# Kernel optimization log

Measured on AMD Instinct MI355X. Metric: run time of the kernel, lower is better.

Reference implementation:

```python
import jax, jax.numpy as jnp
import numpy as np

B, N = 1, 512
NODE_DIM, EDGE_DIM = 384, 128
H, SK, SV, PK, PV = 8, 16, 16, 4, 4
EPS = 1e-8
LN_EPS = 1e-5


def setup_inputs() -> dict:
    key = jax.random.key(0)
    ks = jax.random.split(key, 20)
    d, e = NODE_DIM, EDGE_DIM
    s = 0.02
    rn = lambda k, sh: jax.random.normal(k, sh, jnp.float32) * s
    # orthonormal per-residue rotations (valid rigid frames)
    R, _ = jnp.linalg.qr(jax.random.normal(ks[2], (B, N, 3, 3), jnp.float32))
    out_dim = H * (SV + EDGE_DIM + PV * 4)  # scalar + pairwise + points(3) + point norms(1)
    return dict(
        node_features=jax.random.normal(ks[0], (B, N, d), jnp.float32),
        edge_features=jax.random.normal(ks[1], (B, N, N, e), jnp.float32),
        rotations=R,
        translations=jax.random.normal(ks[3], (B, N, 3), jnp.float32),
        mask=jnp.ones((B, N), bool),
        Wq_s=rn(ks[4], (d, H * SK)), Wk_s=rn(ks[5], (d, H * SK)), Wv_s=rn(ks[6], (d, H * SV)),
        Wq_p=rn(ks[7], (d, H * PK * 3)), Wk_p=rn(ks[8], (d, H * PK * 3)), Wv_p=rn(ks[9], (d, H * PV * 3)),
        point_weights=jnp.full((H,), np.log(np.e - 1.0), jnp.float32),  # softplus -> 1
        Wb=rn(ks[10], (e, H)), bb=jnp.zeros((H,), jnp.float32),
        Wo=rn(ks[11], (out_dim, d)), bo=jnp.zeros((d,), jnp.float32),
        g1=jnp.ones((d,), jnp.float32), beta1=jnp.zeros((d,), jnp.float32),
        W1=rn(ks[12], (d, 2 * d)), b1=jnp.zeros((2 * d,), jnp.float32),
        W2=rn(ks[13], (2 * d, 2 * d)), b2=jnp.zeros((2 * d,), jnp.float32),
        W3=rn(ks[14], (2 * d, d)), b3=jnp.zeros((d,), jnp.float32),
        g2=jnp.ones((d,), jnp.float32), beta2=jnp.zeros((d,), jnp.float32),
    )


def _layer_norm(x, g, b):
    mu = x.mean(-1, keepdims=True)
    var = ((x - mu) ** 2).mean(-1, keepdims=True)
    return (x - mu) * jax.lax.rsqrt(var + LN_EPS) * g + b


def _forward(node_features, edge_features, rotations, translations, mask,
             Wq_s, Wk_s, Wv_s, Wq_p, Wk_p, Wv_p, point_weights, Wb, bb, Wo, bo,
             g1, beta1, W1, b1, W2, b2, W3, b3, g2, beta2):
    b, n, d = node_features.shape
    # num_attn_logits = 3 (scalar + point + pairwise)
    scal_scale = (3 * SK) ** -0.5
    point_scale = (3 * PK * 4.5) ** -0.5
    pair_scale = 3 ** -0.5

    qs = (node_features @ Wq_s).reshape(b, n, H, SK)
    kk = (node_features @ Wk_s).reshape(b, n, H, SK)
    vs = (node_features @ Wv_s).reshape(b, n, H, SV)

    def apply_rigid(p):  # p: (b,n,h,d,3); global = R^T applied per lucidrains einsum + t
        return jnp.einsum('bnhdc,bncr->bnhdr', p, rotations) + translations[:, :, None, None, :]

    qp = apply_rigid((node_features @ Wq_p).reshape(b, n, H, PK, 3))
    kp = apply_rigid((node_features @ Wk_p).reshape(b, n, H, PK, 3))
    vp = apply_rigid((node_features @ Wv_p).reshape(b, n, H, PV, 3))

    logits = jnp.einsum('bihk,bjhk->bhij', qs, kk) * scal_scale

    # point distance term: sum_{d,c} (q-k)^2 = |q|^2 + |k|^2 - 2 q.k (avoids (b,h,i,j,d,3) tensor)
    w = jax.nn.softplus(point_weights)  # (H,)
    q2 = jnp.einsum('bnhdc,bnhdc->bhn', qp, qp)
    k2 = jnp.einsum('bnhdc,bnhdc->bhn', kp, kp)
    cross = jnp.einsum('bihdc,bjhdc->bhij', qp, kp)
    dist = q2[..., :, None] + k2[..., None, :] - 2.0 * cross  # (b,h,i,j)
    logits = logits - 0.5 * point_scale * w[None, :, None, None] * dist

    pair_bias = (jnp.einsum('bije,eh->bhij', edge_features, Wb) + bb[None, :, None, None]) * pair_scale
    logits = logits + pair_bias

    pm = mask[:, None, :, None] & mask[:, None, None, :]  # (b,1,i,j)
    logits = jnp.where(pm, logits, -jnp.finfo(logits.dtype).max)
    attn = jax.nn.softmax(logits, axis=-1)  # (b,h,i,j)

    rs = jnp.einsum('bhij,bjhv->bihv', attn, vs).reshape(b, n, H * SV)
    rp = jnp.einsum('bhij,bije->bihe', attn, edge_features).reshape(b, n, H * EDGE_DIM)
    pts = jnp.einsum('bhij,bjhdc->bihdc', attn, vp)
    # invert rigid: subtract t, apply R (inverse of R^T application)
    local = jnp.einsum('bihdc,birc->bihdr', pts - translations[:, :, None, None, :], rotations)
    norms = jnp.sqrt((local ** 2).sum(-1) + EPS)  # (b,n,H,PV)

    cat = jnp.concatenate([rs, local.reshape(b, n, H * PV * 3), norms.reshape(b, n, H * PV), rp], axis=-1)
    ipa_out = cat @ Wo + bo

    x = _layer_norm(ipa_out, g1, beta1)  # dropout is identity at eval
    x = jax.nn.relu(x @ W1 + b1)
    x = jax.nn.relu(x @ W2 + b2)
    x = x @ W3 + b3
    return _layer_norm(x, g2, beta2)


def reference(node_features, edge_features, rotations, translations, mask,
              Wq_s, Wk_s, Wv_s, Wq_p, Wk_p, Wv_p, point_weights, Wb, bb, Wo, bo,
              g1, beta1, W1, b1, W2, b2, W3, b3, g2, beta2):
    return _forward(node_features, edge_features, rotations, translations, mask,
                    Wq_s, Wk_s, Wv_s, Wq_p, Wk_p, Wv_p, point_weights, Wb, bb, Wo, bo,
                    g1, beta1, W1, b1, W2, b2, W3, b3, g2, beta2)
```

## Files before the change

kernel.cpp:

```cpp
#include <hip/hip_runtime.h>
#include <cstddef>

#define NN 512
#define DD 384
#define EE 128
#define HH 8
#define JSPLIT 16

static constexpr float SCAL_SCALE  = 0.1443375673f;
static constexpr float POINT_SCALE = 0.1360827635f;
static constexpr float PAIR_SCALE  = 0.5773502692f;
static constexpr float LN_EPS = 1e-5f;
static constexpr float EPS    = 1e-8f;

typedef __bf16 bf16x8 __attribute__((ext_vector_type(8)));
typedef float  f32x4  __attribute__((ext_vector_type(4)));

__device__ __forceinline__ unsigned short bf16_bits(float v) {
    union { __bf16 b; unsigned short s; } c; c.b = (__bf16)v; return c.s;
}
__device__ __forceinline__ float bits2f(unsigned u) {
    union { unsigned u; float f; } c; c.u = u; return c.f;
}

__global__ __launch_bounds__(256) void prep_weights_kernel(
    const float* __restrict__ Wo, const float* __restrict__ W1,
    const float* __restrict__ W2, const float* __restrict__ W3,
    const float* __restrict__ Wq_s, const float* __restrict__ Wk_s,
    const float* __restrict__ Wv_s,
    const float* __restrict__ Wq_p, const float* __restrict__ Wk_p,
    const float* __restrict__ Wv_p, const float* __restrict__ nf,
    unsigned short* __restrict__ WoT, unsigned short* __restrict__ W1T,
    unsigned short* __restrict__ W2T, unsigned short* __restrict__ W3T,
    unsigned short* __restrict__ WprojT, unsigned short* __restrict__ nfb)
{
    const int b = blockIdx.x;
    if (b >= 1884) {
        const int idx = (b - 1884) * 1024 + threadIdx.x * 4;
        float4 v = *(const float4*)(nf + idx);
        unsigned lo = bf16_bits(v.x) | ((unsigned)bf16_bits(v.y) << 16);
        unsigned hi = bf16_bits(v.z) | ((unsigned)bf16_bits(v.w) << 16);
        uint2 pk; pk.x = lo; pk.y = hi;
        *(uint2*)(nfb + idx) = pk;
        return;
    }
    const float* W; unsigned short* out;
    int K, N, tile, rowoff = 0;
    if (b < 480)       { W = Wo;   out = WoT;    K = 1280; N = 384; tile = b; }
    else if (b < 768)  { W = W1;   out = W1T;    K = 384;  N = 768; tile = b - 480; }
    else if (b < 1344) { W = W2;   out = W2T;    K = 768;  N = 768; tile = b - 768; }
    else if (b < 1632) { W = W3;   out = W3T;    K = 768;  N = 384; tile = b - 1344; }
    else if (b < 1680) { W = Wq_s; out = WprojT; K = 384;  N = 128; tile = b - 1632; rowoff = 0; }
    else if (b < 1728) { W = Wk_s; out = WprojT; K = 384;  N = 128; tile = b - 1680; rowoff = 128; }
    else if (b < 1776) { W = Wv_s; out = WprojT; K = 384;  N = 128; tile = b - 1728; rowoff = 256; }
    else if (b < 1812) { W = Wq_p; out = WprojT; K = 384;  N = 96;  tile = b - 1776; rowoff = 384; }
    else if (b < 1848) { W = Wk_p; out = WprojT; K = 384;  N = 96;  tile = b - 1812; rowoff = 480; }
    else               { W = Wv_p; out = WprojT; K = 384;  N = 96;  tile = b - 1848; rowoff = 576; }

    const int ntn = N / 32;
    const int n0 = (tile % ntn) * 32, k0 = (tile / ntn) * 32;
    __shared__ float tb[32][33];
    const int tx = threadIdx.x & 31, ty = threadIdx.x >> 5;
    #pragma unroll
    for (int dy = 0; dy < 32; dy += 8)
        tb[ty + dy][tx] = W[(size_t)(k0 + ty + dy) * N + n0 + tx];
    __syncthreads();
    #pragma unroll
    for (int dy = 0; dy < 32; dy += 8)
        out[(size_t)(rowoff + n0 + ty + dy) * K + k0 + tx] = bf16_bits(tb[tx][ty + dy]);
}

template <int K, int NOUT, bool RELU, bool HASB, bool OUTBF>
__global__ __launch_bounds__(256) void gemm_bf16(
    const unsigned short* __restrict__ Xb, const unsigned short* __restrict__ Wt,
    const float* __restrict__ bias, void* __restrict__ Yv)
{
    const int t = threadIdx.x;
    const int w = t >> 6, lane = t & 63;
    const int r = lane & 15, q = lane >> 4;
    const int mt = w >> 1, kh = w & 1;
    const int n0 = blockIdx.x * 16;
    const int m0 = blockIdx.y * 32 + mt * 16;
    constexpr int KH = K / 2;

    const unsigned short* xrow = Xb + (size_t)(m0 + r) * K + kh * KH + q * 8;
    const unsigned short* wrow = Wt + (size_t)(n0 + r) * K + kh * KH + q * 8;

    f32x4 acc = {0.f, 0.f, 0.f, 0.f};
    #pragma unroll 4
    for (int k0 = 0; k0 < KH; k0 += 32) {
        union { uint4 u; bf16x8 v; } au, bu;
        au.u = *(const uint4*)(xrow + k0);
        bu.u = *(const uint4*)(wrow + k0);
        acc = __builtin_amdgcn_mfma_f32_16x16x32_bf16(au.v, bu.v, acc, 0, 0, 0);
    }

    __shared__ float red[2][16][17];
    if (kh == 1) {
        #pragma unroll
        for (int reg = 0; reg < 4; reg++)
            red[mt][q * 4 + reg][r] = acc[reg];
    }
    __syncthreads();
    if (kh == 1) return;

    const int n = n0 + r;
    const float bi = HASB ? bias[n] : 0.f;
    #pragma unroll
    for (int reg = 0; reg < 4; reg++) {
        const int m = m0 + q * 4 + reg;
        float v = acc[reg] + red[mt][q * 4 + reg][r] + bi;
        if (RELU) v = fmaxf(v, 0.f);
        if (OUTBF) ((unsigned short*)Yv)[(size_t)m * NOUT + n] = bf16_bits(v);
        else       ((float*)Yv)[(size_t)m * NOUT + n] = v;
    }
}

__global__ __launch_bounds__(256) void ipa_post_kernel(
    const float* __restrict__ proj_out, const float* __restrict__ rot,
    const float* __restrict__ trans, const float* __restrict__ pw,
    const float* __restrict__ bb,
    unsigned short* __restrict__ Qp, unsigned short* __restrict__ Kp,
    unsigned short* __restrict__ svT)
{
    const int i = blockIdx.x;
    const int t = threadIdx.x;
    __shared__ float outs[672];
    __shared__ float ptg[288];
    __shared__ float q2s[8], k2s[8], pwh[8];

    for (int f = t; f < 672; f += 256) outs[f] = proj_out[(size_t)i * 672 + f];
    if (t < 8) pwh[t] = 0.5f * POINT_SCALE * log1pf(expf(pw[t]));
    __syncthreads();

    for (int f = t; f < 288; f += 256) {
        int which = f / 96, idx = f % 96;
        int hd = idx / 3, r = idx % 3;
        float acc = trans[(size_t)i * 3 + r];
        #pragma unroll
        for (int c = 0; c < 3; c++)
            acc += outs[384 + which * 96 + hd * 3 + c] * rot[(size_t)i * 9 + c * 3 + r];
        ptg[f] = acc;
    }
    __syncthreads();
    if (t < 16) {
        int which = t / 8, h = t % 8;
        float acc = 0.f;
        #pragma unroll
        for (int m = 0; m < 12; m++) {
            float v = ptg[which * 96 + h * 12 + m];
            acc += v * v;
        }
        (which ? k2s : q2s)[h] = acc;
    }
    __syncthreads();

    {
        const int h = t >> 5, d = t & 31;
        float qv, kv;
        if (d < 16)      { qv = outs[h * 16 + d] * SCAL_SCALE; kv = outs[128 + h * 16 + d]; }
        else if (d < 28) { qv = ptg[h * 12 + d - 16] * (2.f * pwh[h]); kv = ptg[96 + h * 12 + d - 16]; }
        else if (d == 28){ qv = -pwh[h] * q2s[h]; kv = 1.f; }
        else if (d == 29){ qv = 1.f; kv = -pwh[h] * k2s[h]; }
        else if (d == 30){ qv = 1.f; kv = bb[h] * PAIR_SCALE; }
        else             { qv = 0.f; kv = 0.f; }
        Qp[((size_t)i * 8 + h) * 32 + d] = bf16_bits(qv);
        Kp[((size_t)i * 8 + h) * 32 + d] = bf16_bits(kv);
    }
    if (t < 128) {
        int h = t >> 4, v = t & 15;
        svT[((size_t)h * 32 + v) * NN + i] = bf16_bits(outs[256 + h * 16 + v]);
    } else if (t < 224) {
        int idx = t - 128, h = idx / 12, m = idx % 12;
        svT[((size_t)h * 32 + 16 + m) * NN + i] = bf16_bits(ptg[192 + idx]);
    } else {
        int idx = t - 224;
        int h = idx >> 2, m = 28 + (idx & 3);
        svT[((size_t)h * 32 + m) * NN + i] = 0;
    }
}

__global__ __launch_bounds__(256) void ipa_fused2(
    const float* __restrict__ edge,
    const unsigned short* __restrict__ Qp, const unsigned short* __restrict__ Kp,
    const unsigned short* __restrict__ svT, const float* __restrict__ Wb,
    float* __restrict__ Opart, float* __restrict__ Mpart, float* __restrict__ Lpart)
{
    const int js = blockIdx.x;
    const int it = blockIdx.y;
    const int i0 = it * 4;
    const int jbase = js * 32;
    const int t = threadIdx.x;
    const int w = t >> 6, lane = t & 63;
    const int r = lane & 15, q = lane >> 4;
    const int L = lane;

    __shared__ float Lqk[32 * 33];
    __shared__ __align__(16) unsigned short P1[40 * 32];
    __shared__ __align__(16) unsigned short P2[72 * 32];
    __shared__ __align__(16) unsigned short wbTl[8 * 136];
    __shared__ __align__(16) unsigned short eT[4 * 128 * 40];

    if (t < 128) {
        float4 a = *(const float4*)&Wb[t * 8];
        float4 b = *(const float4*)&Wb[t * 8 + 4];
        wbTl[0 * 136 + t] = bf16_bits(a.x * PAIR_SCALE);
        wbTl[1 * 136 + t] = bf16_bits(a.y * PAIR_SCALE);
        wbTl[2 * 136 + t] = bf16_bits(a.z * PAIR_SCALE);
        wbTl[3 * 136 + t] = bf16_bits(a.w * PAIR_SCALE);
        wbTl[4 * 136 + t] = bf16_bits(b.x * PAIR_SCALE);
        wbTl[5 * 136 + t] = bf16_bits(b.y * PAIR_SCALE);
        wbTl[6 * 136 + t] = bf16_bits(b.z * PAIR_SCALE);
        wbTl[7 * 136 + t] = bf16_bits(b.w * PAIR_SCALE);
    }

    float2 pf[32];

    bf16x8 aq[2]; bf16x8 bk[2][2];
    #pragma unroll
    for (int hh = 0; hh < 2; hh++) {
        const int h = w * 2 + hh;
        aq[hh] = *(const bf16x8*)&Qp[((size_t)(i0 + (r & 3)) * 8 + h) * 32 + q * 8];
        #pragma unroll
        for (int jt = 0; jt < 2; jt++)
            bk[hh][jt] = *(const bf16x8*)&Kp[((size_t)(jbase + jt * 16 + r) * 8 + h) * 32 + q * 8];
    }

    {
        const float* src = edge + ((size_t)(i0 + w) * 512 + jbase) * 128 + 2 * L;
        #pragma unroll
        for (int s = 0; s < 32; s++)
            pf[s] = *(const float2*)(src + (size_t)s * 128);
    }

    #pragma unroll
    for (int hh = 0; hh < 2; hh++) {
        const int h = w * 2 + hh;
        #pragma unroll
        for (int jt = 0; jt < 2; jt++) {
            f32x4 acc = {0.f, 0.f, 0.f, 0.f};
            acc = __builtin_amdgcn_mfma_f32_16x16x32_bf16(aq[hh], bk[hh][jt], acc, 0, 0, 0);
            if (q == 0) {
                #pragma unroll
                for (int reg = 0; reg < 4; reg++)
                    Lqk[(h * 4 + reg) * 33 + jt * 16 + r] = acc[reg];
            }
        }
    }
    __syncthreads();

    {
        const int il = w;
        const float* ebase = edge + ((size_t)(i0 + il) * 512 + jbase) * 128;
        #pragma unroll
        for (int jt = 0; jt < 2; jt++) {
            f32x4 acc = {0.f, 0.f, 0.f, 0.f};
            #pragma unroll
            for (int kk = 0; kk < 4; kk++) {
                const float* srcb = ebase + (size_t)(jt * 16 + r) * 128 + kk * 32 + q * 8;
                float4 f0 = *(const float4*)srcb;
                float4 f1 = *(const float4*)(srcb + 4);
                union { uint4 u; bf16x8 v; } aE;
                aE.u.x = (unsigned)bf16_bits(f0.x) | ((unsigned)bf16_bits(f0.y) << 16);
                aE.u.y = (unsigned)bf16_bits(f0.z) | ((unsigned)bf16_bits(f0.w) << 16);
                aE.u.z = (unsigned)bf16_bits(f1.x) | ((unsigned)bf16_bits(f1.y) << 16);
                aE.u.w = (unsigned)bf16_bits(f1.z) | ((unsigned)bf16_bits(f1.w) << 16);
                union { uint4 u; bf16x8 v; } bW;
                bW.u = *(const uint4*)&wbTl[(r & 7) * 136 + kk * 32 + q * 8];
                acc = __builtin_amdgcn_mfma_f32_16x16x32_bf16(aE.v, bW.v, acc, 0, 0, 0);
            }
            if (r < 8) {
                #pragma unroll
                for (int reg = 0; reg < 4; reg++)
                    Lqk[(r * 4 + il) * 33 + jt * 16 + q * 4 + reg] += acc[reg];
            }
        }
    }

    {
        #pragma unroll
        for (int c = 0; c < 2; c++) {
            #pragma unroll
            for (int jb = 0; jb < 4; jb++) {
                union { uint4 u; unsigned short sh[8]; } pk;
                #pragma unroll
                for (int u2 = 0; u2 < 8; u2++)
                    pk.sh[u2] = bf16_bits(c ? pf[jb * 8 + u2].y : pf[jb * 8 + u2].x);
                const int jseg = (jb + (L >> 2)) & 3;
                *(uint4*)&eT[w * 5120 + (2 * L + c) * 40 + jseg * 8] = pk.u;
            }
        }
    }
    __syncthreads();

    if (t < 32) {
        const int h = t >> 2, il = t & 3;
        const float* lrow = &Lqk[(h * 4 + il) * 33];
        float lg[32];
        float mx = -1e30f;
        #pragma unroll
        for (int j = 0; j < 32; j++) {
            lg[j] = lrow[j];
            mx = fmaxf(mx, lg[j]);
        }
        float sum = 0.f;
        #pragma unroll
        for (int j = 0; j < 32; j++) { lg[j] = __expf(lg[j] - mx); sum += lg[j]; }
        Mpart[(size_t)(js * 128 + it) * 32 + h * 4 + il] = mx;
        Lpart[(size_t)(js * 128 + it) * 32 + h * 4 + il] = sum;
        unsigned pk[16];
        #pragma unroll
        for (int s = 0; s < 16; s++)
            pk[s] = (unsigned)bf16_bits(lg[2 * s]) | ((unsigned)bf16_bits(lg[2 * s + 1]) << 16);
        uint4* d1 = (uint4*)&P1[((size_t)il * 8 + h) * 32];
        uint4* d2 = (uint4*)&P2[((size_t)h * 8 + il) * 32];
        #pragma unroll
        for (int s = 0; s < 4; s++) {
            uint4 v; v.x = pk[4*s]; v.y = pk[4*s+1]; v.z = pk[4*s+2]; v.w = pk[4*s+3];
            d1[s] = v; d2[s] = v;
        }
    }
    __syncthreads();

    {
        const int il = w;
        union { uint4 u; bf16x8 v; } bP;
        bP.u = *(const uint4*)&P1[((size_t)il * 8 + r) * 32 + q * 8];
        union { uint4 u; bf16x8 v; } aF[8];
        #pragma unroll
        for (int eb = 0; eb < 8; eb++) {
            const int jseg = (q + 2 * eb + (r >> 3)) & 3;
            aF[eb].u = *(const uint4*)&eT[w * 5120 + (eb * 16 + r) * 40 + jseg * 8];
        }
        f32x4 acc[8];
        #pragma unroll
        for (int eb = 0; eb < 8; eb++) {
            f32x4 c = {0.f, 0.f, 0.f, 0.f};
            acc[eb] = __builtin_amdgcn_mfma_f32_16x16x32_bf16(aF[eb].v, bP.v, c, 0, 0, 0);
        }
        float* orw = Opart + (size_t)((js * 128 + it) * 4 + il) * 1248;
        if (r < 8) {
            #pragma unroll
            for (int eb = 0; eb < 8; eb++)
                *(f32x4*)&orw[r * 156 + 28 + eb * 16 + q * 4] = acc[eb];
        }
    }

    #pragma unroll
    for (int hh = 0; hh < 2; hh++) {
        const int h = w * 2 + hh;
        union { uint4 u; bf16x8 v; } aP;
        aP.u = *(const uint4*)&P2[((size_t)h * 8 + r) * 32 + q * 8];
        #pragma unroll
        for (int ct = 0; ct < 2; ct++) {
            union { uint4 u; bf16x8 v; } bS;
            bS.u = *(const uint4*)&svT[((size_t)h * 32 + ct * 16 + r) * 512 + jbase + q * 8];
            f32x4 c = {0.f, 0.f, 0.f, 0.f};
            f32x4 acc = __builtin_amdgcn_mfma_f32_16x16x32_bf16(aP.v, bS.v, c, 0, 0, 0);
            const int cc = ct * 16 + r;
            if (q == 0 && cc < 28) {
                #pragma unroll
                for (int reg = 0; reg < 4; reg++) {
                    const int i = reg;
                    Opart[((size_t)((js * 128 + it) * 4 + i)) * 1248 + h * 156 + cc] = acc[reg];
                }
            }
        }
    }
}

__global__ __launch_bounds__(256) void ipa_merge(
    const float* __restrict__ Opart, const float* __restrict__ Mpart,
    const float* __restrict__ Lpart, const float* __restrict__ rot,
    const float* __restrict__ trans, unsigned short* __restrict__ cat_bf)
{
    const int i = blockIdx.x;
    const int itile = i >> 2, il = i & 3;
    const int t = threadIdx.x;
    __shared__ float wn[8 * JSPLIT];
    __shared__ float pts_s[96];

    if (t < 8) {
        const int h = t;
        float ms[JSPLIT], ls[JSPLIT], M = -1e30f;
        #pragma unroll
        for (int s = 0; s < JSPLIT; s++) {
            ms[s] = Mpart[(size_t)(s * 128 + itile) * 32 + h * 4 + il];
            ls[s] = Lpart[(size_t)(s * 128 + itile) * 32 + h * 4 + il];
            M = fmaxf(M, ms[s]);
        }
        float denom = 0.f, e[JSPLIT];
        #pragma unroll
        for (int s = 0; s < JSPLIT; s++) { e[s] = __expf(ms[s] - M); denom += e[s] * ls[s]; }
        const float inv = 1.f / denom;
        #pragma unroll
        for (int s = 0; s < JSPLIT; s++) wn[h * JSPLIT + s] = e[s] * inv;
    }
    __syncthreads();

    for (int col = t; col < 1248; col += 256) {
        const int h = col / 156, c = col % 156;
        float acc = 0.f;
        #pragma unroll
        for (int s = 0; s < JSPLIT; s++)
            acc += wn[h * JSPLIT + s] *
                   Opart[((size_t)(s * 128 + itile) * 4 + il) * 1248 + col];
        if (c < 16)      cat_bf[(size_t)i * 1280 + h * 16 + c] = bf16_bits(acc);
        else if (c < 28) pts_s[h * 12 + (c - 16)] = acc;
        else             cat_bf[(size_t)i * 1280 + 256 + h * 128 + (c - 28)] = bf16_bits(acc);
    }
    __syncthreads();

    const float* tr = trans + (size_t)i * 3;
    const float* R  = rot + (size_t)i * 9;
    if (t < 96) {
        int hd = t / 3, rr = t % 3;
        float acc = 0.f;
        #pragma unroll
        for (int c = 0; c < 3; c++)
            acc += (pts_s[hd * 3 + c] - tr[c]) * R[rr * 3 + c];
        cat_bf[(size_t)i * 1280 + 128 + t] = bf16_bits(acc);
    } else if (t < 128) {
        int pv = t - 96;
        float s = EPS;
        #pragma unroll
        for (int rr = 0; rr < 3; rr++) {
            float v = 0.f;
            #pragma unroll
            for (int c = 0; c < 3; c++)
                v += (pts_s[pv * 3 + c] - tr[c]) * R[rr * 3 + c];
            s += v * v;
        }
        cat_bf[(size_t)i * 1280 + 224 + pv] = bf16_bits(sqrtf(s));
    }
}

template <bool OUTBF>
__global__ __launch_bounds__(256) void ln_kernel(
    const float* __restrict__ X, const float* __restrict__ g,
    const float* __restrict__ beta, void* __restrict__ Yv, int Dim)
{
    __shared__ float red[4];
    __shared__ float bc;
    const int i = blockIdx.x;
    const int t = threadIdx.x;
    const float* x = X + (size_t)i * Dim;

    float s = 0.f;
    for (int k = t; k < Dim; k += 256) s += x[k];
    #pragma unroll
    for (int off = 32; off; off >>= 1) s += __shfl_down(s, off, 64);
    if ((t & 63) == 0) red[t >> 6] = s;
    __syncthreads();
    if (t == 0) bc = red[0] + red[1] + red[2] + red[3];
    __syncthreads();
    const float mu = bc / Dim;

    float v = 0.f;
    for (int k = t; k < Dim; k += 256) { float d = x[k] - mu; v += d * d; }
    #pragma unroll
    for (int off = 32; off; off >>= 1) v += __shfl_down(v, off, 64);
    __syncthreads();
    if ((t & 63) == 0) red[t >> 6] = v;
    __syncthreads();
    if (t == 0) bc = red[0] + red[1] + red[2] + red[3];
    __syncthreads();
    const float rstd = rsqrtf(bc / Dim + LN_EPS);

    for (int k = t; k < Dim; k += 256) {
        float val = (x[k] - mu) * rstd * g[k] + beta[k];
        if (OUTBF) ((unsigned short*)Yv)[(size_t)i * Dim + k] = bf16_bits(val);
        else       ((float*)Yv)[(size_t)i * Dim + k] = val;
    }
}

extern "C" void kernel_launch(void* const* d_in, const int* in_sizes, int n_in,
                              void* d_out, int out_size, void* d_ws, size_t ws_size,
                              hipStream_t stream)
{
    const float* nf    = (const float*)d_in[0];
    const float* edge  = (const float*)d_in[1];
    const float* rot   = (const float*)d_in[2];
    const float* trans = (const float*)d_in[3];
    const float* Wq_s = (const float*)d_in[5];
    const float* Wk_s = (const float*)d_in[6];
    const float* Wv_s = (const float*)d_in[7];
    const float* Wq_p = (const float*)d_in[8];
    const float* Wk_p = (const float*)d_in[9];
    const float* Wv_p = (const float*)d_in[10];
    const float* pw   = (const float*)d_in[11];
    const float* Wb   = (const float*)d_in[12];
    const float* bb   = (const float*)d_in[13];
    const float* Wo   = (const float*)d_in[14];
    const float* bo   = (const float*)d_in[15];
    const float* g1   = (const float*)d_in[16];
    const float* be1  = (const float*)d_in[17];
    const float* W1   = (const float*)d_in[18];
    const float* b1   = (const float*)d_in[19];
    const float* W2   = (const float*)d_in[20];
    const float* b2   = (const float*)d_in[21];
    const float* W3   = (const float*)d_in[22];
    const float* b3   = (const float*)d_in[23];
    const float* g2   = (const float*)d_in[24];
    const float* be2  = (const float*)d_in[25];

    float* ws = (float*)d_ws;
    float* proj_out = ws;
    float* ipa   = proj_out + 344064;
    float* y     = ipa + 196608;
    float* Opart = y + 196608;
    float* Mpart = Opart + 10223616;
    float* Lpart = Mpart + 65536;
    unsigned short* cat_bf = (unsigned short*)(Lpart + 65536);
    unsigned short* x1b = cat_bf + 655360;
    unsigned short* h1b = x1b + 196608;
    unsigned short* h2b = h1b + 393216;
    unsigned short* Qp  = h2b + 393216;
    unsigned short* Kp  = Qp + 131072;
    unsigned short* svT = Kp + 131072;
    unsigned short* WoT = svT + 131072;
    unsigned short* W1T = WoT + 491520;
    unsigned short* W2T = W1T + 294912;
    unsigned short* W3T = W2T + 589824;
    unsigned short* WprojT = W3T + 294912;
    unsigned short* nfb = WprojT + 258048;

    prep_weights_kernel<<<2076, 256, 0, stream>>>(Wo, W1, W2, W3,
                                                  Wq_s, Wk_s, Wv_s, Wq_p, Wk_p, Wv_p, nf,
                                                  WoT, W1T, W2T, W3T, WprojT, nfb);

    gemm_bf16<384, 672, false, false, false><<<dim3(42, 16), 256, 0, stream>>>(nfb, WprojT, nullptr, proj_out);

    ipa_post_kernel<<<NN, 256, 0, stream>>>(proj_out, rot, trans, pw, bb, Qp, Kp, svT);

    ipa_fused2<<<dim3(JSPLIT, 128), 256, 0, stream>>>(edge, Qp, Kp, svT, Wb,
                                                      Opart, Mpart, Lpart);

    ipa_merge<<<NN, 256, 0, stream>>>(Opart, Mpart, Lpart, rot, trans, cat_bf);

    gemm_bf16<1280, 384, false, true, false><<<dim3(24, 16), 256, 0, stream>>>(cat_bf, WoT, bo, ipa);
    ln_kernel<true><<<NN, 256, 0, stream>>>(ipa, g1, be1, x1b, 384);

    gemm_bf16<384, 768, true, true, true><<<dim3(48, 16), 256, 0, stream>>>(x1b, W1T, b1, h1b);
    gemm_bf16<768, 768, true, true, true><<<dim3(48, 16), 256, 0, stream>>>(h1b, W2T, b2, h2b);
    gemm_bf16<768, 384, false, true, false><<<dim3(24, 16), 256, 0, stream>>>(h2b, W3T, b3, y);

    ln_kernel<false><<<NN, 256, 0, stream>>>(y, g2, be2, d_out, 384);
}
```

Baseline: 320.9 us.

## Halve query rows per attention block and split edge work across wave pairs

The fused IPA attention kernel now handles 2 query rows per block instead of 4 and doubles the grid to 256 row tiles. Each pair of waves shares one row, and the edge-bias and edge-aggregation MFMAs are split by j-tile or e-half. This lowers per-thread register use (pf shrinks from float2[32] to float[32]) and shared memory, to raise occupancy and block count. In exchange, Q/K loads and Wb staging are repeated across twice as many blocks, the QK MFMA wastes more of its tile, and the merge indexing has to change to match.

```diff
diff --git a/kernel.cpp b/kernel.cpp
--- a/kernel.cpp
+++ b/kernel.cpp
@@ -188,18 +188,19 @@
 {
     const int js = blockIdx.x;
     const int it = blockIdx.y;
-    const int i0 = it * 4;
+    const int i0 = it * 2;
     const int jbase = js * 32;
     const int t = threadIdx.x;
     const int w = t >> 6, lane = t & 63;
     const int r = lane & 15, q = lane >> 4;
     const int L = lane;
-
-    __shared__ float Lqk[32 * 33];
-    __shared__ __align__(16) unsigned short P1[40 * 32];
+    const int sw = w & 1, eh = w >> 1;
+
+    __shared__ float Lqk[16 * 33];
+    __shared__ __align__(16) unsigned short P1[24 * 32];
     __shared__ __align__(16) unsigned short P2[72 * 32];
     __shared__ __align__(16) unsigned short wbTl[8 * 136];
-    __shared__ __align__(16) unsigned short eT[4 * 128 * 40];
+    __shared__ __align__(16) unsigned short eT[2 * 128 * 40];
 
     if (t < 128) {
         float4 a = *(const float4*)&Wb[t * 8];
@@ -214,23 +215,24 @@
         wbTl[7 * 136 + t] = bf16_bits(b.w * PAIR_SCALE);
     }
 
-    float2 pf[32];
+    float pf[32];
 
     bf16x8 aq[2]; bf16x8 bk[2][2];
     #pragma unroll
     for (int hh = 0; hh < 2; hh++) {
         const int h = w * 2 + hh;
-        aq[hh] = *(const bf16x8*)&Qp[((size_t)(i0 + (r & 3)) * 8 + h) * 32 + q * 8];
+        aq[hh] = *(const bf16x8*)&Qp[((size_t)(i0 + (r & 1)) * 8 + h) * 32 + q * 8];
         #pragma unroll
         for (int jt = 0; jt < 2; jt++)
             bk[hh][jt] = *(const bf16x8*)&Kp[((size_t)(jbase + jt * 16 + r) * 8 + h) * 32 + q * 8];
     }
 
+    const int ecol = eh * 64 + L;
     {
-        const float* src = edge + ((size_t)(i0 + w) * 512 + jbase) * 128 + 2 * L;
+        const float* src = edge + ((size_t)(i0 + sw) * 512 + jbase) * 128 + ecol;
         #pragma unroll
         for (int s = 0; s < 32; s++)
-            pf[s] = *(const float2*)(src + (size_t)s * 128);
+            pf[s] = src[(size_t)s * 128];
     }
 
     #pragma unroll
@@ -242,60 +244,54 @@
             acc = __builtin_amdgcn_mfma_f32_16x16x32_bf16(aq[hh], bk[hh][jt], acc, 0, 0, 0);
             if (q == 0) {
                 #pragma unroll
-                for (int reg = 0; reg < 4; reg++)
-                    Lqk[(h * 4 + reg) * 33 + jt * 16 + r] = acc[reg];
+                for (int reg = 0; reg < 2; reg++)
+                    Lqk[(h * 2 + reg) * 33 + jt * 16 + r] = acc[reg];
             }
         }
     }
     __syncthreads();
 
     {
-        const int il = w;
+        const int il = sw, jt = eh;
         const float* ebase = edge + ((size_t)(i0 + il) * 512 + jbase) * 128;
-        #pragma unroll
-        for (int jt = 0; jt < 2; jt++) {
-            f32x4 acc = {0.f, 0.f, 0.f, 0.f};
+        f32x4 acc = {0.f, 0.f, 0.f, 0.f};
+        #pragma unroll
+        for (int kk = 0; kk < 4; kk++) {
+            const float* srcb = ebase + (size_t)(jt * 16 + r) * 128 + kk * 32 + q * 8;
+            float4 f0 = *(const float4*)srcb;
+            float4 f1 = *(const float4*)(srcb + 4);
+            union { uint4 u; bf16x8 v; } aE;
+            aE.u.x = (unsigned)bf16_bits(f0.x) | ((unsigned)bf16_bits(f0.y) << 16);
+            aE.u.y = (unsigned)bf16_bits(f0.z) | ((unsigned)bf16_bits(f0.w) << 16);
+            aE.u.z = (unsigned)bf16_bits(f1.x) | ((unsigned)bf16_bits(f1.y) << 16);
+            aE.u.w = (unsigned)bf16_bits(f1.z) | ((unsigned)bf16_bits(f1.w) << 16);
+            union { uint4 u; bf16x8 v; } bW;
+            bW.u = *(const uint4*)&wbTl[(r & 7) * 136 + kk * 32 + q * 8];
+            acc = __builtin_amdgcn_mfma_f32_16x16x32_bf16(aE.v, bW.v, acc, 0, 0, 0);
+        }
+        if (r < 8) {
             #pragma unroll
-            for (int kk = 0; kk < 4; kk++) {
-                const float* srcb = ebase + (size_t)(jt * 16 + r) * 128 + kk * 32 + q * 8;
-                float4 f0 = *(const float4*)srcb;
-                float4 f1 = *(const float4*)(srcb + 4);
-                union { uint4 u; bf16x8 v; } aE;
-                aE.u.x = (unsigned)bf16_bits(f0.x) | ((unsigned)bf16_bits(f0.y) << 16);
-                aE.u.y = (unsigned)bf16_bits(f0.z) | ((unsigned)bf16_bits(f0.w) << 16);
-                aE.u.z = (unsigned)bf16_bits(f1.x) | ((unsigned)bf16_bits(f1.y) << 16);
-                aE.u.w = (unsigned)bf16_bits(f1.z) | ((unsigned)bf16_bits(f1.w) << 16);
-                union { uint4 u; bf16x8 v; } bW;
-                bW.u = *(const uint4*)&wbTl[(r & 7) * 136 + kk * 32 + q * 8];
-                acc = __builtin_amdgcn_mfma_f32_16x16x32_bf16(aE.v, bW.v, acc, 0, 0, 0);
-            }
-            if (r < 8) {
-                #pragma unroll
-                for (int reg = 0; reg < 4; reg++)
-                    Lqk[(r * 4 + il) * 33 + jt * 16 + q * 4 + reg] += acc[reg];
-            }
+            for (int reg = 0; reg < 4; reg++)
+                Lqk[(r * 2 + il) * 33 + jt * 16 + q * 4 + reg] += acc[reg];
         }
     }
 
     {
         #pragma unroll
-        for (int c = 0; c < 2; c++) {
+        for (int jb = 0; jb < 4; jb++) {
+            union { uint4 u; unsigned short sh[8]; } pk;
             #pragma unroll
-            for (int jb = 0; jb < 4; jb++) {
-                union { uint4 u; unsigned short sh[8]; } pk;
-                #pragma unroll
-                for (int u2 = 0; u2 < 8; u2++)
-                    pk.sh[u2] = bf16_bits(c ? pf[jb * 8 + u2].y : pf[jb * 8 + u2].x);
-                const int jseg = (jb + (L >> 2)) & 3;
-                *(uint4*)&eT[w * 5120 + (2 * L + c) * 40 + jseg * 8] = pk.u;
-            }
-        }
-    }
-    __syncthreads();
-
-    if (t < 32) {
-        const int h = t >> 2, il = t & 3;
-        const float* lrow = &Lqk[(h * 4 + il) * 33];
+            for (int u2 = 0; u2 < 8; u2++)
+                pk.sh[u2] = bf16_bits(pf[jb * 8 + u2]);
+            const int jseg = (jb + (ecol >> 3)) & 3;
+            *(uint4*)&eT[sw * 5120 + ecol * 40 + jseg * 8] = pk.u;
+        }
+    }
+    __syncthreads();
+
+    if (t < 16) {
+        const int h = t >> 1, il = t & 1;
+        const float* lrow = &Lqk[(h * 2 + il) * 33];
         float lg[32];
         float mx = -1e30f;
         #pragma unroll
@@ -306,8 +302,8 @@
         float sum = 0.f;
         #pragma unroll
         for (int j = 0; j < 32; j++) { lg[j] = __expf(lg[j] - mx); sum += lg[j]; }
-        Mpart[(size_t)(js * 128 + it) * 32 + h * 4 + il] = mx;
-        Lpart[(size_t)(js * 128 + it) * 32 + h * 4 + il] = sum;
+        Mpart[(size_t)(js * 256 + it) * 16 + h * 2 + il] = mx;
+        Lpart[(size_t)(js * 256 + it) * 16 + h * 2 + il] = sum;
         unsigned pk[16];
         #pragma unroll
         for (int s = 0; s < 16; s++)
@@ -323,26 +319,29 @@
     __syncthreads();
 
     {
-        const int il = w;
+        const int il = sw;
         union { uint4 u; bf16x8 v; } bP;
         bP.u = *(const uint4*)&P1[((size_t)il * 8 + r) * 32 + q * 8];
-        union { uint4 u; bf16x8 v; } aF[8];
-        #pragma unroll
-        for (int eb = 0; eb < 8; eb++) {
+        union { uint4 u; bf16x8 v; } aF[4];
+        #pragma unroll
+        for (int e4 = 0; e4 < 4; e4++) {
+            const int eb = eh * 4 + e4;
             const int jseg = (q + 2 * eb + (r >> 3)) & 3;
-            aF[eb].u = *(const uint4*)&eT[w * 5120 + (eb * 16 + r) * 40 + jseg * 8];
-        }
-        f32x4 acc[8];
-        #pragma unroll
-        for (int eb = 0; eb < 8; eb++) {
+            aF[e4].u = *(const uint4*)&eT[sw * 5120 + (eb * 16 + r) * 40 + jseg * 8];
+        }
+        f32x4 acc[4];
+        #pragma unroll
+        for (int e4 = 0; e4 < 4; e4++) {
             f32x4 c = {0.f, 0.f, 0.f, 0.f};
-            acc[eb] = __builtin_amdgcn_mfma_f32_16x16x32_bf16(aF[eb].v, bP.v, c, 0, 0, 0);
-        }
-        float* orw = Opart + (size_t)((js * 128 + it) * 4 + il) * 1248;
+            acc[e4] = __builtin_amdgcn_mfma_f32_16x16x32_bf16(aF[e4].v, bP.v, c, 0, 0, 0);
+        }
+        float* orw = Opart + (size_t)((js * 256 + it) * 2 + il) * 1248;
         if (r < 8) {
             #pragma unroll
-            for (int eb = 0; eb < 8; eb++)
-                *(f32x4*)&orw[r * 156 + 28 + eb * 16 + q * 4] = acc[eb];
+            for (int e4 = 0; e4 < 4; e4++) {
+                const int eb = eh * 4 + e4;
+                *(f32x4*)&orw[r * 156 + 28 + eb * 16 + q * 4] = acc[e4];
+            }
         }
     }
 
@@ -360,10 +359,8 @@
             const int cc = ct * 16 + r;
             if (q == 0 && cc < 28) {
                 #pragma unroll
-                for (int reg = 0; reg < 4; reg++) {
-                    const int i = reg;
-                    Opart[((size_t)((js * 128 + it) * 4 + i)) * 1248 + h * 156 + cc] = acc[reg];
-                }
+                for (int reg = 0; reg < 2; reg++)
+                    Opart[((size_t)((js * 256 + it) * 2 + reg)) * 1248 + h * 156 + cc] = acc[reg];
             }
         }
     }
@@ -375,7 +372,7 @@
     const float* __restrict__ trans, unsigned short* __restrict__ cat_bf)
 {
     const int i = blockIdx.x;
-    const int itile = i >> 2, il = i & 3;
+    const int itile = i >> 1, il = i & 1;
     const int t = threadIdx.x;
     __shared__ float wn[8 * JSPLIT];
     __shared__ float pts_s[96];
@@ -385,8 +382,8 @@
         float ms[JSPLIT], ls[JSPLIT], M = -1e30f;
         #pragma unroll
         for (int s = 0; s < JSPLIT; s++) {
-            ms[s] = Mpart[(size_t)(s * 128 + itile) * 32 + h * 4 + il];
-            ls[s] = Lpart[(size_t)(s * 128 + itile) * 32 + h * 4 + il];
+            ms[s] = Mpart[(size_t)(s * 256 + itile) * 16 + h * 2 + il];
+            ls[s] = Lpart[(size_t)(s * 256 + itile) * 16 + h * 2 + il];
             M = fmaxf(M, ms[s]);
         }
         float denom = 0.f, e[JSPLIT];
@@ -404,7 +401,7 @@
         #pragma unroll
         for (int s = 0; s < JSPLIT; s++)
             acc += wn[h * JSPLIT + s] *
-                   Opart[((size_t)(s * 128 + itile) * 4 + il) * 1248 + col];
+                   Opart[((size_t)(s * 256 + itile) * 2 + il) * 1248 + col];
         if (c < 16)      cat_bf[(size_t)i * 1280 + h * 16 + c] = bf16_bits(acc);
         else if (c < 28) pts_s[h * 12 + (c - 16)] = acc;
         else             cat_bf[(size_t)i * 1280 + 256 + h * 128 + (c - 28)] = bf16_bits(acc);
@@ -533,7 +530,7 @@
 
     ipa_post_kernel<<<NN, 256, 0, stream>>>(proj_out, rot, trans, pw, bb, Qp, Kp, svT);
 
-    ipa_fused2<<<dim3(JSPLIT, 128), 256, 0, stream>>>(edge, Qp, Kp, svT, Wb,
+    ipa_fused2<<<dim3(JSPLIT, 256), 256, 0, stream>>>(edge, Qp, Kp, svT, Wb,
                                                       Opart, Mpart, Lpart);
 
     ipa_merge<<<NN, 256, 0, stream>>>(Opart, Mpart, Lpart, rot, trans, cat_bf);
```

Measured after the change: 322.3 us. Within noise of the previous version (+0.4%).
